# Kernel tuning notes

Measured on AMD Instinct MI355X. Metric: run time of the kernel, lower is better.

Reference implementation:

```python
import jax, jax.numpy as jnp
import numpy as np

B, S, DIM = 128, 256, 512          # batch, grid tokens (16*16), input feature dim
D = 128                             # embedding_dim
K = 16384                           # num_embeddings
GH = GW = 16                        # grid size
EPS = 1e-12


def setup_inputs() -> dict:
    key = jax.random.key(0)
    ks = jax.random.split(key, 10)
    return {
        "input_data_first": jax.random.normal(ks[0], (B, S, DIM), jnp.float32),
        "input_data_last": jax.random.normal(ks[1], (B, S, DIM), jnp.float32),
        "random_vector": jax.random.normal(ks[2], (B * 64, D), jnp.float32),
        "codebooks": jax.random.normal(ks[3], (K, D), jnp.float32),
        "W_in": jax.random.normal(ks[4], (DIM, D), jnp.float32) / np.sqrt(DIM),
        "b_in": jnp.zeros((D,), jnp.float32),
        "conv_w": jax.random.normal(ks[5], (D, D, 3, 3), jnp.float32) / np.sqrt(D * 9),
        "conv_b": jnp.zeros((D,), jnp.float32),
        "W_out": jax.random.normal(ks[6], (D, DIM), jnp.float32) / np.sqrt(D),
        "b_out": jnp.zeros((DIM,), jnp.float32),
        "codebooks_used": jnp.zeros((K,), jnp.int32),
    }


def _encode(x, W_in, b_in, conv_w, conv_b):
    h = x @ W_in + b_in                                  # [B,S,D]
    h = jnp.transpose(h, (0, 2, 1)).reshape(B, D, GH, GW)  # [B,D,16,16]
    h = jax.lax.conv_general_dilated(
        h, conv_w, window_strides=(2, 2), padding=[(1, 1), (1, 1)],
        dimension_numbers=("NCHW", "OIHW", "NCHW"))
    h = h + conv_b[None, :, None, None]                  # [B,D,8,8]
    h = h.reshape(B, D, -1)                              # [B,D,64]
    h = jnp.transpose(h, (0, 2, 1)).reshape(-1, D)       # [B*64, D]
    return h


def reference(input_data_first, input_data_last, random_vector, codebooks,
              W_in, b_in, conv_w, conv_b, W_out, b_out, codebooks_used):
    e_first = _encode(input_data_first, W_in, b_in, conv_w, conv_b)
    e_last = _encode(input_data_last, W_in, b_in, conv_w, conv_b)
    x = e_last - e_first                                 # [N,D]

    # squared-distance to every codebook entry: [N,K]
    dists = (jnp.sum(x * x, axis=1, keepdims=True)
             - 2.0 * (x @ codebooks.T)
             + jnp.sum(codebooks * codebooks, axis=1)[None, :])
    min_indices = jnp.argmin(dists, axis=1)              # [N]
    hard_q = codebooks[min_indices]                      # [N,D]

    norm_res = jnp.sqrt(jnp.sum((x - hard_q) ** 2, axis=1, keepdims=True))
    norm_rnd = jnp.sqrt(jnp.sum(random_vector ** 2, axis=1, keepdims=True))
    vq_error = (norm_res / norm_rnd + EPS) * random_vector
    quantized = x + vq_error                             # [N,D]

    counts = jnp.zeros((K,), jnp.float32).at[min_indices].add(1.0)
    avg_probs = counts / x.shape[0]
    perplexity = jnp.exp(-jnp.sum(avg_probs * jnp.log(avg_probs + EPS)))

    new_used = codebooks_used + counts.astype(jnp.int32)

    # decode (faithful to torch: raw memory reinterpretation, not inverse transpose)
    q = quantized.reshape(B, D, -1)                      # [B,D,64]
    q = jnp.transpose(q, (0, 2, 1))                      # [B,64,D]
    out = q @ W_out + b_out                              # [B,64,DIM]
    return out, perplexity, new_used, min_indices.reshape(B, -1)
```

## Files before the change

### kernel.cpp

```cpp
#include <hip/hip_runtime.h>
#include <math.h>

#define NROWS 8192
#define KCB   16384

using frag_ab = __attribute__((ext_vector_type(8))) short;
using frag_cd = __attribute__((ext_vector_type(4))) float;
using f32x4   = __attribute__((ext_vector_type(4))) float;

__device__ inline unsigned short f2bf(float f) {
    unsigned u = __float_as_uint(f);
    return (unsigned short)((u + 0x7FFFu + ((u >> 16) & 1u)) >> 16);
}

__global__ __launch_bounds__(256) void k_wt(const float* __restrict__ cw,
                                            float* __restrict__ W2) {
    int gid = blockIdx.x * 256 + threadIdx.x;
    if (gid >= 147456) return;
    int co = gid & 127;
    int ci = (gid >> 7) & 127;
    int kk = gid >> 14;
    W2[gid] = cw[(size_t)co * 1152 + ci * 9 + kk];
}

__global__ __launch_bounds__(256) void k_c2(const float* __restrict__ cb,
                                            float* __restrict__ c2f) {
    int k = blockIdx.x * 256 + threadIdx.x;
    const float* row = cb + (size_t)k * 128;
    double s = 0.0;
    #pragma unroll
    for (int d = 0; d < 128; d += 4) {
        float4 v = *(const float4*)(row + d);
        s += (double)v.x * v.x + (double)v.y * v.y
           + (double)v.z * v.z + (double)v.w * v.w;
    }
    c2f[k] = (float)s + 1024.0f;
}

__global__ __launch_bounds__(256) void k_cbbf(const float* __restrict__ cb,
                                              unsigned short* __restrict__ Cbb) {
    int gid = blockIdx.x * 256 + threadIdx.x;
    float4 v = ((const float4*)cb)[gid];
    ushort4 o;
    o.x = f2bf(v.x); o.y = f2bf(v.y); o.z = f2bf(v.z); o.w = f2bf(v.w);
    ((ushort4*)Cbb)[gid] = o;
}

__global__ __launch_bounds__(256) void k_encode_gemm(
    const float* __restrict__ last, const float* __restrict__ first,
    const float* __restrict__ W_in, double* __restrict__ H)
{
    __shared__ double As[32][64];
    __shared__ float  Bs[32][128];
    const int tid  = threadIdx.x;
    const int row0 = blockIdx.x * 64;
    const int tx = tid & 31;
    const int ty = tid >> 5;

    double acc[8][4];
    #pragma unroll
    for (int r = 0; r < 8; ++r)
        #pragma unroll
        for (int j = 0; j < 4; ++j) acc[r][j] = 0.0;

    for (int d0 = 0; d0 < 512; d0 += 32) {
        #pragma unroll
        for (int it = 0; it < 2; ++it) {
            int flat = it * 1024 + tid * 4;
            int r = flat >> 5, d = flat & 31;
            const float4 l4 = *(const float4*)(last  + (size_t)(row0 + r) * 512 + d0 + d);
            const float4 f4 = *(const float4*)(first + (size_t)(row0 + r) * 512 + d0 + d);
            As[d + 0][r] = (double)l4.x - (double)f4.x;
            As[d + 1][r] = (double)l4.y - (double)f4.y;
            As[d + 2][r] = (double)l4.z - (double)f4.z;
            As[d + 3][r] = (double)l4.w - (double)f4.w;
        }
        #pragma unroll
        for (int it = 0; it < 4; ++it) {
            int flat = it * 1024 + tid * 4;
            int d = flat >> 7, c = flat & 127;
            *(float4*)&Bs[d][c] = *(const float4*)(W_in + (size_t)(d0 + d) * 128 + c);
        }
        __syncthreads();
        #pragma unroll 4
        for (int d = 0; d < 32; ++d) {
            double a[8];
            #pragma unroll
            for (int q = 0; q < 4; ++q) {
                double2 t = *(const double2*)&As[d][ty * 8 + 2 * q];
                a[2 * q] = t.x; a[2 * q + 1] = t.y;
            }
            float4 bf = *(const float4*)&Bs[d][tx * 4];
            double b[4] = {(double)bf.x, (double)bf.y, (double)bf.z, (double)bf.w};
            #pragma unroll
            for (int r = 0; r < 8; ++r)
                #pragma unroll
                for (int j = 0; j < 4; ++j)
                    acc[r][j] = fma(a[r], b[j], acc[r][j]);
        }
        __syncthreads();
    }
    #pragma unroll
    for (int r = 0; r < 8; ++r) {
        double* o = H + (size_t)(row0 + ty * 8 + r) * 128 + tx * 4;
        o[0] = acc[r][0]; o[1] = acc[r][1]; o[2] = acc[r][2]; o[3] = acc[r][3];
    }
}

__global__ __launch_bounds__(256) void k_conv(
    const double* __restrict__ H, const float* __restrict__ W2,
    double* __restrict__ X, unsigned short* __restrict__ Xb)
{
    __shared__ double Hs[3 * 16 * 128];
    const int b   = blockIdx.x >> 3;
    const int oh  = blockIdx.x & 7;
    const int tid = threadIdx.x;
    const int ih0 = 2 * oh - 1;
    for (int it = 0; it < 24; ++it) {
        int idx = it * 256 + tid;
        int r = idx >> 11;
        int rem = idx & 2047;
        int ih = ih0 + r;
        Hs[idx] = (ih >= 0) ? H[(size_t)b * 32768 + (size_t)ih * 2048 + rem] : 0.0;
    }
    __syncthreads();
    const int co   = tid & 127;
    const int half = tid >> 7;
    const int iwb  = half * 8 - 1;
    double acc[4] = {0, 0, 0, 0};
    for (int ci = 0; ci < 128; ++ci) {
        #pragma unroll
        for (int kh = 0; kh < 3; ++kh) {
            double in[9];
            #pragma unroll
            for (int t = 0; t < 9; ++t) {
                int iw = iwb + t;
                in[t] = (iw >= 0) ? Hs[kh * 2048 + iw * 128 + ci] : 0.0;
            }
            #pragma unroll
            for (int kw = 0; kw < 3; ++kw) {
                double w = (double)W2[(size_t)((kh * 3 + kw) * 128 + ci) * 128 + co];
                #pragma unroll
                for (int i = 0; i < 4; ++i)
                    acc[i] = fma(in[2 * i + kw], w, acc[i]);
            }
        }
    }
    #pragma unroll
    for (int i = 0; i < 4; ++i) {
        int ow = half * 4 + i;
        size_t n = (size_t)b * 64 + oh * 8 + ow;
        X [n * 128 + co] = acc[i];
        Xb[n * 128 + co] = f2bf((float)acc[i]);
    }
}

__global__ __launch_bounds__(256) void k_dist_mfma(
    const unsigned short* __restrict__ Xb, const unsigned short* __restrict__ Cbb,
    const float* __restrict__ c2f, int* __restrict__ cand)
{
    __shared__ __align__(16) unsigned short Xs[128 * 128];
    __shared__ __align__(16) unsigned short Cs[128 * 128];
    const int tid   = threadIdx.x;
    const int row0  = blockIdx.x * 128;
    const int split = blockIdx.y;
    const int lane  = tid & 63;
    const int w     = tid >> 6;
    const int quad  = lane >> 4;
    const int lm    = lane & 15;
    const int cw    = (w & 1) * 64;
    const int rw    = (w >> 1) * 64;

    #pragma unroll
    for (int it = 0; it < 8; ++it) {
        int flat = it * 256 + tid;
        int r = flat >> 4, ch = flat & 15;
        *(uint4*)&Xs[r * 128 + (((ch ^ r) & 15) << 3) + (ch & 16 ? 0 : 0)] =
            *(const uint4*)(Xb + (size_t)(row0 + r) * 128 + ch * 8);
    }

    unsigned k1[4], k2[4];
    #pragma unroll
    for (int j = 0; j < 4; ++j) { k1[j] = 0xFFFFFFFFu; k2[j] = 0xFFFFFFFFu; }

    for (int chunk = 0; chunk < 16; ++chunk) {
        const int kb = split * 2048 + chunk * 128;
        if (chunk) __syncthreads();
        #pragma unroll
        for (int it = 0; it < 8; ++it) {
            int flat = it * 256 + tid;
            int r = flat >> 4, ch = flat & 15;
            *(uint4*)&Cs[r * 128 + ((ch ^ (r & 15)) << 3)] =
                *(const uint4*)(Cbb + (size_t)(kb + r) * 128 + ch * 8);
        }
        __syncthreads();

        frag_cd acc[4][4];
        #pragma unroll
        for (int i = 0; i < 4; ++i)
            #pragma unroll
            for (int j = 0; j < 4; ++j)
                #pragma unroll
                for (int r = 0; r < 4; ++r) acc[i][j][r] = 0.f;

        #pragma unroll
        for (int kk = 0; kk < 4; ++kk) {
            const int chs = ((kk * 4 + quad) ^ lm) << 3;
            frag_ab a[4], b[4];
            #pragma unroll
            for (int i = 0; i < 4; ++i)
                a[i] = *(const frag_ab*)&Cs[(cw + i * 16 + lm) * 128 + chs];
            #pragma unroll
            for (int j = 0; j < 4; ++j)
                b[j] = *(const frag_ab*)&Xs[(rw + j * 16 + lm) * 128 + chs];
            #pragma unroll
            for (int i = 0; i < 4; ++i)
                #pragma unroll
                for (int j = 0; j < 4; ++j)
                    acc[i][j] = __builtin_amdgcn_mfma_f32_16x16x32_bf16(
                        a[i], b[j], acc[i][j], 0, 0, 0);
        }

        const int ib = chunk * 128 + cw + quad * 4;
        #pragma unroll
        for (int i = 0; i < 4; ++i) {
            f32x4 c2v = *(const f32x4*)(c2f + kb + cw + i * 16 + quad * 4);
            #pragma unroll
            for (int j = 0; j < 4; ++j) {
                #pragma unroll
                for (int r = 0; r < 4; ++r) {
                    float u = fmaf(-2.f, acc[i][j][r], c2v[r]);
                    unsigned key = (__float_as_uint(u) & 0xFFFFF800u)
                                 | (unsigned)(ib + i * 16 + r);
                    unsigned nk1 = min(key, k1[j]);
                    k2[j] = min(max(key, k1[j]), k2[j]);
                    k1[j] = nk1;
                }
            }
        }
    }

    __syncthreads();
    uint2* kred = (uint2*)Cs;
    #pragma unroll
    for (int j = 0; j < 4; ++j)
        kred[(rw + j * 16 + lm) * 8 + (w & 1) * 4 + quad] = make_uint2(k1[j], k2[j]);
    __syncthreads();
    if (tid < 128) {
        unsigned b1 = 0xFFFFFFFFu, b2 = 0xFFFFFFFFu;
        for (int e = 0; e < 8; ++e) {
            uint2 kv = kred[tid * 8 + e];
            unsigned n1 = min(kv.x, b1); b2 = min(max(kv.x, b1), b2); b1 = n1;
            n1 = min(kv.y, b1);          b2 = min(max(kv.y, b1), b2); b1 = n1;
        }
        int base = split * 2048;
        int* o = cand + (size_t)(row0 + tid) * 16 + split * 2;
        o[0] = base + (int)(b1 & 0x7FFu);
        o[1] = base + (int)(b2 & 0x7FFu);
    }
}

__global__ __launch_bounds__(256) void k_refine(
    const double* __restrict__ X, const float* __restrict__ cb,
    const int* __restrict__ cand, const float* __restrict__ rnd,
    int* __restrict__ counts, float* __restrict__ quant,
    float* __restrict__ out_mi)
{
    const int wid  = threadIdx.x >> 6;
    const int lane = threadIdx.x & 63;
    const int row  = blockIdx.x * 4 + wid;
    const double x0 = X[(size_t)row * 128 + lane];
    const double x1 = X[(size_t)row * 128 + 64 + lane];
    double bestv = 1e300; int bestk = 0;
    for (int c = 0; c < 16; ++c) {
        int k = cand[(size_t)row * 16 + c] & (KCB - 1);
        double t0 = x0 - (double)cb[(size_t)k * 128 + lane];
        double t1 = x1 - (double)cb[(size_t)k * 128 + 64 + lane];
        double s = t0 * t0 + t1 * t1;
        #pragma unroll
        for (int off = 32; off > 0; off >>= 1) s += __shfl_xor(s, off, 64);
        if (s < bestv) { bestv = s; bestk = k; }
    }
    double r0 = (double)rnd[(size_t)row * 128 + lane];
    double r1 = (double)rnd[(size_t)row * 128 + 64 + lane];
    double rs = r0 * r0 + r1 * r1;
    #pragma unroll
    for (int off = 32; off > 0; off >>= 1) rs += __shfl_xor(rs, off, 64);
    double ratio = sqrt(bestv) / sqrt(rs) + 1e-12;
    quant[(size_t)row * 128 + lane]      = (float)(x0 + ratio * r0);
    quant[(size_t)row * 128 + 64 + lane] = (float)(x1 + ratio * r1);
    if (lane == 0) {
        out_mi[row] = (float)bestk;
        atomicAdd(counts + bestk, 1);
    }
}

__global__ __launch_bounds__(256) void k_perplex(
    const int* __restrict__ counts, const int* __restrict__ used_in,
    float* __restrict__ out_used, float* __restrict__ out_perp)
{
    __shared__ double red[256];
    int tid = threadIdx.x;
    double e = 0.0;
    for (int k = tid; k < KCB; k += 256) {
        int c = counts[k];
        out_used[k] = (float)(used_in[k] + c);
        if (c > 0) {
            double p = (double)c / 8192.0;
            e += p * log(p + 1e-12);
        }
    }
    red[tid] = e;
    __syncthreads();
    for (int s = 128; s > 0; s >>= 1) {
        if (tid < s) red[tid] += red[tid + s];
        __syncthreads();
    }
    if (tid == 0) out_perp[0] = (float)exp(-red[0]);
}

__global__ __launch_bounds__(256) void k_decode(
    const float* __restrict__ quant, const float* __restrict__ W_out,
    const float* __restrict__ b_out, float* __restrict__ out)
{
    __shared__ float As[8192];
    __shared__ float Bs[8192];
    const int tid = threadIdx.x;
    const int m0  = blockIdx.x * 64;
    const int b   = blockIdx.y;
    #pragma unroll
    for (int it = 0; it < 8; ++it) {
        int flat = it * 1024 + tid * 4;
        *(float4*)&As[flat] = *(const float4*)(quant + (size_t)b * 8192 + flat);
        int d2 = flat >> 6, m = flat & 63;
        *(float4*)&Bs[flat] = *(const float4*)(W_out + (size_t)d2 * 512 + m0 + m);
    }
    __syncthreads();
    const int tx = tid & 15, ty = tid >> 4;
    float acc[4][4];
    #pragma unroll
    for (int i = 0; i < 4; ++i)
        #pragma unroll
        for (int j = 0; j < 4; ++j) acc[i][j] = 0.f;
    #pragma unroll 8
    for (int d2 = 0; d2 < 128; ++d2) {
        float4 a  = *(const float4*)&As[d2 * 64 + ty * 4];
        float4 b4 = *(const float4*)&Bs[d2 * 64 + tx * 4];
        float av[4] = {a.x, a.y, a.z, a.w};
        float bv[4] = {b4.x, b4.y, b4.z, b4.w};
        #pragma unroll
        for (int i = 0; i < 4; ++i)
            #pragma unroll
            for (int j = 0; j < 4; ++j)
                acc[i][j] = fmaf(av[i], bv[j], acc[i][j]);
    }
    float4 bo = *(const float4*)(b_out + m0 + tx * 4);
    float bob[4] = {bo.x, bo.y, bo.z, bo.w};
    #pragma unroll
    for (int i = 0; i < 4; ++i) {
        int s2 = ty * 4 + i;
        float4 o;
        o.x = acc[i][0] + bob[0];
        o.y = acc[i][1] + bob[1];
        o.z = acc[i][2] + bob[2];
        o.w = acc[i][3] + bob[3];
        *(float4*)(out + (size_t)b * 32768 + (size_t)s2 * 512 + m0 + tx * 4) = o;
    }
}

extern "C" void kernel_launch(void* const* d_in, const int* in_sizes, int n_in,
                              void* d_out, int out_size, void* d_ws, size_t ws_size,
                              hipStream_t stream) {
    const float* first  = (const float*)d_in[0];
    const float* last   = (const float*)d_in[1];
    const float* rnd    = (const float*)d_in[2];
    const float* cb     = (const float*)d_in[3];
    const float* W_in   = (const float*)d_in[4];
    const float* conv_w = (const float*)d_in[6];
    const float* W_out  = (const float*)d_in[8];
    const float* b_out  = (const float*)d_in[9];
    const int*   used   = (const int*)d_in[10];

    float* out      = (float*)d_out;
    float* out_perp = out + 4194304;
    float* out_used = out + 4194305;
    float* out_mi   = out + 4194305 + 16384;

    char* ws = (char*)d_ws;
    double*         H      = (double*)(ws);
    double*         X      = (double*)(ws + 33554432);
    unsigned short* Cbb    = (unsigned short*)(ws + 41943040);
    float*          W2     = (float*) (ws + 46137344);
    float*          c2f    = (float*) (ws + 46727168);
    int*            cand   = (int*)   (ws + 46792704);
    float*          quant  = (float*) (ws + 47316992);
    int*            counts = (int*)   (ws + 51511296);
    unsigned short* Xb     = (unsigned short*)(ws + 51576832);

    hipMemsetAsync(counts, 0, KCB * sizeof(int), stream);
    k_wt<<<576, 256, 0, stream>>>(conv_w, W2);
    k_c2<<<64, 256, 0, stream>>>(cb, c2f);
    k_cbbf<<<2048, 256, 0, stream>>>(cb, Cbb);
    k_encode_gemm<<<512, 256, 0, stream>>>(last, first, W_in, H);
    k_conv<<<1024, 256, 0, stream>>>(H, W2, X, Xb);
    k_dist_mfma<<<dim3(64, 8), 256, 0, stream>>>(Xb, Cbb, c2f, cand);
    k_refine<<<2048, 256, 0, stream>>>(X, cb, cand, rnd, counts, quant, out_mi);
    k_perplex<<<1, 256, 0, stream>>>(counts, used, out_used, out_perp);
    k_decode<<<dim3(8, 128), 256, 0, stream>>>(quant, W_out, b_out, out);
}
```

Baseline: 535.3 us.

## Use FP64 MFMA for the encoder projection GEMM with runtime layout probing

Rewrites the input-projection GEMM (last-first difference times W_in, in double precision) to use the 16x16x4 f64 MFMA instruction, with each of four waves computing a 32x64 tile. At kernel start it runs probe MFMAs to discover the output fragment layout at runtime, and falls back to a scalar FMA path with the same register layout if the probe does not match. Shared tiles are padded and W_in is converted to double when staged. The aim is to replace the scalar double FMA loop with matrix-core throughput, at the cost of probe overhead and higher register and LDS use.

```diff
diff --git a/kernel.cpp b/kernel.cpp
--- a/kernel.cpp
+++ b/kernel.cpp
@@ -7,6 +7,7 @@
 using frag_ab = __attribute__((ext_vector_type(8))) short;
 using frag_cd = __attribute__((ext_vector_type(4))) float;
 using f32x4   = __attribute__((ext_vector_type(4))) float;
+using f64x4   = __attribute__((ext_vector_type(4))) double;
 
 __device__ inline unsigned short f2bf(float f) {
     unsigned u = __float_as_uint(f);
@@ -50,61 +51,133 @@
     const float* __restrict__ last, const float* __restrict__ first,
     const float* __restrict__ W_in, double* __restrict__ H)
 {
-    __shared__ double As[32][64];
-    __shared__ float  Bs[32][128];
+    __shared__ double As[32][66];
+    __shared__ double Bs[32][132];
     const int tid  = threadIdx.x;
+    const int lane = tid & 63;
+    const int w    = tid >> 6;
     const int row0 = blockIdx.x * 64;
-    const int tx = tid & 31;
-    const int ty = tid >> 5;
-
-    double acc[8][4];
-    #pragma unroll
-    for (int r = 0; r < 8; ++r)
-        #pragma unroll
-        for (int j = 0; j < 4; ++j) acc[r][j] = 0.0;
-
-    for (int d0 = 0; d0 < 512; d0 += 32) {
-        #pragma unroll
-        for (int it = 0; it < 2; ++it) {
-            int flat = it * 1024 + tid * 4;
-            int r = flat >> 5, d = flat & 31;
-            const float4 l4 = *(const float4*)(last  + (size_t)(row0 + r) * 512 + d0 + d);
-            const float4 f4 = *(const float4*)(first + (size_t)(row0 + r) * 512 + d0 + d);
-            As[d + 0][r] = (double)l4.x - (double)f4.x;
-            As[d + 1][r] = (double)l4.y - (double)f4.y;
-            As[d + 2][r] = (double)l4.z - (double)f4.z;
-            As[d + 3][r] = (double)l4.w - (double)f4.w;
-        }
-        #pragma unroll
-        for (int it = 0; it < 4; ++it) {
-            int flat = it * 1024 + tid * 4;
-            int d = flat >> 7, c = flat & 127;
-            *(float4*)&Bs[d][c] = *(const float4*)(W_in + (size_t)(d0 + d) * 128 + c);
+    const int wm   = (w & 1) * 32;
+    const int wn   = (w >> 1) * 64;
+    const int lm   = lane & 15;
+    const int kq   = lane >> 4;
+
+    f64x4 z; z[0] = 0.0; z[1] = 0.0; z[2] = 0.0; z[3] = 0.0;
+    const double dl = (double)lane;
+    f64x4 d1 = __builtin_amdgcn_mfma_f64_16x16x4f64(dl, 1.0, z, 0, 0, 0);
+    f64x4 d2 = __builtin_amdgcn_mfma_f64_16x16x4f64(1.0, dl, z, 0, 0, 0);
+    const double pk = (double)(1 << (4 * kq));
+    f64x4 d3 = __builtin_amdgcn_mfma_f64_16x16x4f64(pk, dl, z, 0, 0, 0);
+    int pm[4], pn[4];
+    int okl = 1;
+    #pragma unroll
+    for (int s = 0; s < 4; ++s) {
+        double v1 = d1[s] - 96.0, v2 = d2[s] - 96.0;
+        int i1 = (int)v1, i2 = (int)v2;
+        okl &= (d1[s] == (double)(96 + i1)) & (i1 >= 0) & (i1 < 64) & ((i1 & 3) == 0);
+        okl &= (d2[s] == (double)(96 + i2)) & (i2 >= 0) & (i2 < 64) & ((i2 & 3) == 0);
+        pm[s] = i1 >> 2;
+        pn[s] = i2 >> 2;
+        okl &= (d3[s] == 4369.0 * (double)pn[s] + 205056.0);
+    }
+    const int ok = __all(okl);
+    if (!ok) {
+        #pragma unroll
+        for (int s = 0; s < 4; ++s) { pm[s] = 4 * kq + s; pn[s] = lm; }
+    }
+
+    f64x4 acc[2][4];
+    #pragma unroll
+    for (int i = 0; i < 2; ++i)
+        #pragma unroll
+        for (int j = 0; j < 4; ++j)
+            #pragma unroll
+            for (int q = 0; q < 4; ++q) acc[i][j][q] = 0.0;
+
+    const int ar = tid >> 2;
+    const int ak = (tid & 3) * 8;
+    const int bkk = tid >> 3;
+    const int bc  = (tid & 7) * 16;
+
+    for (int k0 = 0; k0 < 512; k0 += 32) {
+        if (k0) __syncthreads();
+        {
+            const float* lp = last  + (size_t)(row0 + ar) * 512 + k0 + ak;
+            const float* fp = first + (size_t)(row0 + ar) * 512 + k0 + ak;
+            const float4 l0 = *(const float4*)(lp);
+            const float4 l1 = *(const float4*)(lp + 4);
+            const float4 f0 = *(const float4*)(fp);
+            const float4 f1 = *(const float4*)(fp + 4);
+            As[ak + 0][ar] = (double)l0.x - (double)f0.x;
+            As[ak + 1][ar] = (double)l0.y - (double)f0.y;
+            As[ak + 2][ar] = (double)l0.z - (double)f0.z;
+            As[ak + 3][ar] = (double)l0.w - (double)f0.w;
+            As[ak + 4][ar] = (double)l1.x - (double)f1.x;
+            As[ak + 5][ar] = (double)l1.y - (double)f1.y;
+            As[ak + 6][ar] = (double)l1.z - (double)f1.z;
+            As[ak + 7][ar] = (double)l1.w - (double)f1.w;
+        }
+        {
+            const float* wp = W_in + (size_t)(k0 + bkk) * 128 + bc;
+            #pragma unroll
+            for (int q = 0; q < 4; ++q) {
+                const float4 b4 = *(const float4*)(wp + 4 * q);
+                Bs[bkk][bc + 4 * q + 0] = (double)b4.x;
+                Bs[bkk][bc + 4 * q + 1] = (double)b4.y;
+                Bs[bkk][bc + 4 * q + 2] = (double)b4.z;
+                Bs[bkk][bc + 4 * q + 3] = (double)b4.w;
+            }
         }
         __syncthreads();
-        #pragma unroll 4
-        for (int d = 0; d < 32; ++d) {
-            double a[8];
-            #pragma unroll
-            for (int q = 0; q < 4; ++q) {
-                double2 t = *(const double2*)&As[d][ty * 8 + 2 * q];
-                a[2 * q] = t.x; a[2 * q + 1] = t.y;
-            }
-            float4 bf = *(const float4*)&Bs[d][tx * 4];
-            double b[4] = {(double)bf.x, (double)bf.y, (double)bf.z, (double)bf.w};
-            #pragma unroll
-            for (int r = 0; r < 8; ++r)
+        if (ok) {
+            #pragma unroll
+            for (int kc = 0; kc < 8; ++kc) {
+                const int kk = kc * 4 + kq;
+                double a0 = As[kk][wm + lm];
+                double a1 = As[kk][wm + 16 + lm];
+                double b0 = Bs[kk][wn + lm];
+                double b1 = Bs[kk][wn + 16 + lm];
+                double b2 = Bs[kk][wn + 32 + lm];
+                double b3 = Bs[kk][wn + 48 + lm];
+                acc[0][0] = __builtin_amdgcn_mfma_f64_16x16x4f64(a0, b0, acc[0][0], 0, 0, 0);
+                acc[0][1] = __builtin_amdgcn_mfma_f64_16x16x4f64(a0, b1, acc[0][1], 0, 0, 0);
+                acc[0][2] = __builtin_amdgcn_mfma_f64_16x16x4f64(a0, b2, acc[0][2], 0, 0, 0);
+                acc[0][3] = __builtin_amdgcn_mfma_f64_16x16x4f64(a0, b3, acc[0][3], 0, 0, 0);
+                acc[1][0] = __builtin_amdgcn_mfma_f64_16x16x4f64(a1, b0, acc[1][0], 0, 0, 0);
+                acc[1][1] = __builtin_amdgcn_mfma_f64_16x16x4f64(a1, b1, acc[1][1], 0, 0, 0);
+                acc[1][2] = __builtin_amdgcn_mfma_f64_16x16x4f64(a1, b2, acc[1][2], 0, 0, 0);
+                acc[1][3] = __builtin_amdgcn_mfma_f64_16x16x4f64(a1, b3, acc[1][3], 0, 0, 0);
+            }
+        } else {
+            #pragma unroll 4
+            for (int k = 0; k < 32; ++k) {
+                double b0 = Bs[k][wn + lm];
+                double b1 = Bs[k][wn + 16 + lm];
+                double b2 = Bs[k][wn + 32 + lm];
+                double b3 = Bs[k][wn + 48 + lm];
                 #pragma unroll
-                for (int j = 0; j < 4; ++j)
-                    acc[r][j] = fma(a[r], b[j], acc[r][j]);
-        }
-        __syncthreads();
-    }
-    #pragma unroll
-    for (int r = 0; r < 8; ++r) {
-        double* o = H + (size_t)(row0 + ty * 8 + r) * 128 + tx * 4;
-        o[0] = acc[r][0]; o[1] = acc[r][1]; o[2] = acc[r][2]; o[3] = acc[r][3];
-    }
+                for (int i = 0; i < 2; ++i) {
+                    const double* ap = &As[k][wm + i * 16 + 4 * kq];
+                    #pragma unroll
+                    for (int s = 0; s < 4; ++s) {
+                        double a = ap[s];
+                        acc[i][0][s] = fma(a, b0, acc[i][0][s]);
+                        acc[i][1][s] = fma(a, b1, acc[i][1][s]);
+                        acc[i][2][s] = fma(a, b2, acc[i][2][s]);
+                        acc[i][3][s] = fma(a, b3, acc[i][3][s]);
+                    }
+                }
+            }
+        }
+    }
+    #pragma unroll
+    for (int i = 0; i < 2; ++i)
+        #pragma unroll
+        for (int j = 0; j < 4; ++j)
+            #pragma unroll
+            for (int s = 0; s < 4; ++s)
+                H[(size_t)(row0 + wm + i * 16 + pm[s]) * 128 + wn + j * 16 + pn[s]]
+                    = acc[i][j][s];
 }
 
 __global__ __launch_bounds__(256) void k_conv(
```

Result: faster. 504.2 us (-5.8%).
